# Performance work log

Measured on AMD Instinct MI355X. Metric: run time of the kernel, lower is better.

## Reference

```python
import jax, jax.numpy as jnp
import numpy as np

QMIN, QMAX = 0.0, 255.0  # uint8 activation quantization range


def _qlinear(x, w_q, b, s_in, zp_in, s_w):
    """zentorch_qlinear: quantize fp32 x to uint8, int8 weight, dequant output.

    x:   [M, K] fp32
    w_q: [N, K] int8 values (stored int32), symmetric (weight zp = 0)
    b:   [N] fp32
    s_in, zp_in: scalars (activation scale / zero point)
    s_w: [N] per-output-channel weight scales
    """
    zp = zp_in.astype(jnp.float32)
    q = jnp.clip(jnp.round(x / s_in) + zp, QMIN, QMAX)      # fake-quant uint8
    x_dq = (q - zp) * s_in                                   # dequantized activation
    w_dq = w_q.astype(jnp.float32) * s_w[:, None]            # [N, K] dequant weight
    return x_dq @ w_dq.T + b                                 # [M, N] fp32


def setup_inputs() -> dict:
    key = jax.random.key(0)
    k1, k2, k3, k4 = jax.random.split(key, 4)
    M, K, N = 8192, 4096, 4096
    inp = {
        "input": jax.random.normal(k1, (M, K), dtype=jnp.float32),
        "weights": jax.random.randint(k2, (N, K), -128, 128, dtype=jnp.int32),
        "biases": jax.random.normal(k3, (N,), dtype=jnp.float32) * 0.1,
        "input_scales": jnp.array([0.05], dtype=jnp.float32),
        "input_zero_points": jnp.array([128], dtype=jnp.int32),
        "weight_scales": jax.random.uniform(k4, (N,), dtype=jnp.float32, minval=0.001, maxval=0.01),
        "weight_zero_points": jnp.zeros((N,), dtype=jnp.int32),
        "output_dtype": 0,  # 0 -> float32
    }
    return inp


def reference(input, weights, biases, input_scales, input_zero_points,
              weight_scales, weight_zero_points, output_dtype):
    s_in = input_scales[0]
    zp_in = input_zero_points[0]
    x = _qlinear(input, weights, biases, s_in, zp_in, weight_scales)
    x = _qlinear(x, weights, biases, s_in, zp_in, weight_scales)
    x = _qlinear(x, weights, biases, s_in, zp_in, weight_scales)
    return x
```

## Files before the change

kernel.cpp:

```cpp
#include <hip/hip_runtime.h>
#include <stdint.h>

#define M_DIM 8192
#define K_DIM 4096
#define N_DIM 4096
#define KTILES (K_DIM / 64)

typedef __attribute__((ext_vector_type(4))) int i32x4;

__global__ void pack_w_kernel(const int* __restrict__ w, char* __restrict__ wp,
                              int* __restrict__ corr, const int* __restrict__ zpp) {
  __shared__ int red[256];
  const int n = blockIdx.x;
  const int t = threadIdx.x;
  const int4* row = (const int4*)(w + (size_t)n * K_DIM);
  int s = 0;
  int words[4];
#pragma unroll
  for (int u = 0; u < 4; ++u) {
    int4 v = row[t * 4 + u];
    s += v.x + v.y + v.z + v.w;
    words[u] = (v.x & 255) | ((v.y & 255) << 8) | ((v.z & 255) << 16) | (v.w << 24);
  }
  ((int4*)(wp + (size_t)n * K_DIM))[t] = make_int4(words[0], words[1], words[2], words[3]);
  red[t] = s;
  __syncthreads();
  for (int off = 128; off > 0; off >>= 1) {
    if (t < off) red[t] += red[t + off];
    __syncthreads();
  }
  if (t == 0) corr[n] = (128 - zpp[0]) * red[0];
}

__global__ void quant_in_kernel(const float* __restrict__ x, char* __restrict__ q,
                                const float* __restrict__ sp, const int* __restrict__ zpp) {
  const int i = blockIdx.x * blockDim.x + threadIdx.x;
  const float s = sp[0];
  const float zp = (float)zpp[0];
  float4 v = ((const float4*)x)[i];
  float t0 = fminf(fmaxf(rintf(v.x / s) + zp, 0.f), 255.f);
  float t1 = fminf(fmaxf(rintf(v.y / s) + zp, 0.f), 255.f);
  float t2 = fminf(fmaxf(rintf(v.z / s) + zp, 0.f), 255.f);
  float t3 = fminf(fmaxf(rintf(v.w / s) + zp, 0.f), 255.f);
  int b0 = (int)t0 - 128, b1 = (int)t1 - 128, b2 = (int)t2 - 128, b3 = (int)t3 - 128;
  ((int*)q)[i] = (b0 & 255) | ((b1 & 255) << 8) | ((b2 & 255) << 16) | (b3 << 24);
}

#define STAGE16(SRC, DST)                                                     \
  __builtin_amdgcn_global_load_lds(                                           \
      (const __attribute__((address_space(1))) void*)(SRC),                   \
      (__attribute__((address_space(3))) void*)(DST), 16, 0, 0)

#define RD(p) (*(const i32x4*)(p))

#define BAR __builtin_amdgcn_s_barrier()
#define LGKM0 asm volatile("s_waitcnt lgkmcnt(0)" ::: "memory")
#define SCHED0 __builtin_amdgcn_sched_barrier(0)

#define MF8(I0, AV, J0, BV)                                                   \
  _Pragma("unroll") for (int i_ = 0; i_ < 4; ++i_)                            \
      _Pragma("unroll") for (int j_ = 0; j_ < 2; ++j_)                        \
          acc[(I0) + i_][(J0) + j_] = __builtin_amdgcn_mfma_i32_16x16x64_i8(  \
              AV[i_], BV[j_], acc[(I0) + i_][(J0) + j_], 0, 0, 0);

#define TILE8(SLOT, KSTG)                                                     \
  {                                                                           \
    const char* sA_ = &lds[SLOT][0][0];                                       \
    const char* sB_ = &lds[SLOT][1][0];                                       \
    char* nA_ = &lds[((SLOT) + 3) & 3][0][0];                                 \
    char* nB_ = &lds[((SLOT) + 3) & 3][1][0];                                 \
    i32x4 aL[4], aH[4], bL[2], bH[2];                                         \
                                             \
    _Pragma("unroll") for (int i_ = 0; i_ < 4; ++i_)                          \
        aL[i_] = RD(sA_ + aoff[i_]);                                          \
    bL[0] = RD(sB_ + boff[0]);                                                \
    bL[1] = RD(sB_ + boff[1]);                                                \
    STAGE16(asrc0 + (size_t)(KSTG), nA_ + o0_);                               \
    BAR; LGKM0; SCHED0;                                                       \
    __builtin_amdgcn_s_setprio(1); MF8(0, aL, 0, bL)                          \
    __builtin_amdgcn_s_setprio(0);                                            \
    BAR;                                                                      \
                                             \
    bH[0] = RD(sB_ + boff[2]);                                                \
    bH[1] = RD(sB_ + boff[3]);                                                \
    STAGE16(asrc1 + (size_t)(KSTG), nA_ + o1_);                               \
    BAR; LGKM0; SCHED0;                                                       \
    __builtin_amdgcn_s_setprio(1); MF8(0, aL, 2, bH)                          \
    __builtin_amdgcn_s_setprio(0);                                            \
    BAR;                                                                      \
                                             \
    _Pragma("unroll") for (int i_ = 0; i_ < 4; ++i_)                          \
        aH[i_] = RD(sA_ + aoff[4 + i_]);                                      \
    STAGE16(bsrc0 + (size_t)(KSTG), nB_ + o0_);                               \
    BAR; LGKM0; SCHED0;                                                       \
    __builtin_amdgcn_s_setprio(1); MF8(4, aH, 2, bH)                          \
    __builtin_amdgcn_s_setprio(0);                                            \
    BAR;                                                                      \
                                  \
    STAGE16(bsrc1 + (size_t)(KSTG), nB_ + o1_);                               \
    BAR; SCHED0;                                                              \
    __builtin_amdgcn_s_setprio(1); MF8(4, aH, 0, bL)                          \
    __builtin_amdgcn_s_setprio(0);                                            \
    asm volatile("s_waitcnt vmcnt(8)" ::: "memory");                          \
    BAR;                                                                      \
  }

template <int WRITE_Q>
__global__ __launch_bounds__(512, 2) void gemm_kernel(
    const char* __restrict__ qa, const char* __restrict__ wb,
    const int* __restrict__ corr, const float* __restrict__ swp,
    const float* __restrict__ bias, const float* __restrict__ sp,
    const int* __restrict__ zpp, char* __restrict__ outq, float* __restrict__ outf) {
  __shared__ __align__(16) char lds[4][2][16384];
  const int tid = threadIdx.x;
  const int lane = tid & 63;
  const int w = tid >> 6;
  const int wr = w >> 2;
  const int wc = w & 3;
  const int bid = blockIdx.x;
  const int bm = bid & 31;
  const int bn = bid >> 5;
  const char* abase = qa + (size_t)bm * 256 * K_DIM;
  const char* bbase = wb + (size_t)bn * 256 * K_DIM;

  const int o0_ = tid * 16;
  const int o1_ = 8192 + tid * 16;
  const int r0_ = o0_ >> 6, r1_ = o1_ >> 6;
  const int g0_ = ((o0_ >> 4) & 3) ^ ((r0_ >> 1) & 3);
  const int g1_ = ((o1_ >> 4) & 3) ^ ((r1_ >> 1) & 3);
  const char* asrc0 = abase + (size_t)r0_ * K_DIM + g0_ * 16;
  const char* asrc1 = abase + (size_t)r1_ * K_DIM + g1_ * 16;
  const int p0_ = (r0_ & ~63) + 4 * (r0_ & 15) + ((r0_ >> 4) & 3);
  const int p1_ = (r1_ & ~63) + 4 * (r1_ & 15) + ((r1_ >> 4) & 3);
  const char* bsrc0 = bbase + (size_t)p0_ * K_DIM + g0_ * 16;
  const char* bsrc1 = bbase + (size_t)p1_ * K_DIM + g1_ * 16;

  const int rr = lane & 15;
  const int g = lane >> 4;
  int aoff[8], boff[4];
#pragma unroll
  for (int i = 0; i < 8; ++i) {
    const int row = wr * 128 + i * 16 + rr;
    aoff[i] = (row << 6) + ((g ^ ((row >> 1) & 3)) << 4);
  }
#pragma unroll
  for (int j = 0; j < 4; ++j) {
    const int row = wc * 64 + j * 16 + rr;
    boff[j] = (row << 6) + ((g ^ ((row >> 1) & 3)) << 4);
  }

  i32x4 acc[8][4] = {};

  STAGE16(asrc0, &lds[0][0][o0_]); STAGE16(asrc1, &lds[0][0][o1_]);
  STAGE16(bsrc0, &lds[0][1][o0_]); STAGE16(bsrc1, &lds[0][1][o1_]);
  STAGE16(asrc0 + 64, &lds[1][0][o0_]); STAGE16(asrc1 + 64, &lds[1][0][o1_]);
  STAGE16(bsrc0 + 64, &lds[1][1][o0_]); STAGE16(bsrc1 + 64, &lds[1][1][o1_]);
  STAGE16(asrc0 + 128, &lds[2][0][o0_]); STAGE16(asrc1 + 128, &lds[2][0][o1_]);
  STAGE16(bsrc0 + 128, &lds[2][1][o0_]); STAGE16(bsrc1 + 128, &lds[2][1][o1_]);
  asm volatile("s_waitcnt vmcnt(8)" ::: "memory");
  __builtin_amdgcn_s_barrier();

  for (int tb = 0; tb < KTILES / 4; ++tb) {
#pragma unroll
    for (int u = 0; u < 4; ++u) {
      const int t = tb * 4 + u;
      const int ks_ = (t + 3 < KTILES ? t + 3 : KTILES - 1) * 64;
      TILE8(u, ks_);
    }
  }
  asm volatile("s_waitcnt vmcnt(0)" ::: "memory");

  const float s = sp[0];
  const float zpf = (float)zpp[0];
  const int m0 = bm * 256 + wr * 128 + (lane >> 4) * 4;
  const int nb4 = bn * 256 + wc * 64 + ((lane & 15) << 2);
  const int4 cr4 = *(const int4*)(corr + nb4);
  const float4 sw4 = *(const float4*)(swp + nb4);
  const float4 bb4 = *(const float4*)(bias + nb4);
  const float fs0 = s * sw4.x, fs1 = s * sw4.y, fs2 = s * sw4.z, fs3 = s * sw4.w;
#pragma unroll
  for (int i = 0; i < 8; ++i) {
#pragma unroll
    for (int q = 0; q < 4; ++q) {
      const int m = m0 + i * 16 + q;
      const float v0 = fs0 * (float)(acc[i][0][q] + cr4.x) + bb4.x;
      const float v1 = fs1 * (float)(acc[i][1][q] + cr4.y) + bb4.y;
      const float v2 = fs2 * (float)(acc[i][2][q] + cr4.z) + bb4.z;
      const float v3 = fs3 * (float)(acc[i][3][q] + cr4.w) + bb4.w;
      if (WRITE_Q) {
        const int b0i = (int)fminf(fmaxf(rintf(v0 / s) + zpf, 0.f), 255.f) - 128;
        const int b1i = (int)fminf(fmaxf(rintf(v1 / s) + zpf, 0.f), 255.f) - 128;
        const int b2i = (int)fminf(fmaxf(rintf(v2 / s) + zpf, 0.f), 255.f) - 128;
        const int b3i = (int)fminf(fmaxf(rintf(v3 / s) + zpf, 0.f), 255.f) - 128;
        const uint32_t pk = (uint32_t)(b0i & 255) | ((uint32_t)(b1i & 255) << 8) |
                            ((uint32_t)(b2i & 255) << 16) | ((uint32_t)b3i << 24);
        *(uint32_t*)(outq + (size_t)m * N_DIM + nb4) = pk;
      } else {
        float4 o4;
        o4.x = v0; o4.y = v1; o4.z = v2; o4.w = v3;
        *(float4*)(outf + (size_t)m * N_DIM + nb4) = o4;
      }
    }
  }
}

extern "C" void kernel_launch(void* const* d_in, const int* in_sizes, int n_in,
                              void* d_out, int out_size, void* d_ws, size_t ws_size,
                              hipStream_t stream) {
  const float* x = (const float*)d_in[0];
  const int* wq = (const int*)d_in[1];
  const float* bias = (const float*)d_in[2];
  const float* s_in = (const float*)d_in[3];
  const int* zp_in = (const int*)d_in[4];
  const float* s_w = (const float*)d_in[5];
  float* out = (float*)d_out;

  const size_t WP_BYTES = (size_t)N_DIM * K_DIM;
  const size_t Q_BYTES = (size_t)M_DIM * K_DIM;
  char* ws = (char*)d_ws;
  char* wp = ws;
  char* q1 = ws + WP_BYTES;
  char* q2 = q1 + Q_BYTES;
  int* corr = (int*)(q2 + Q_BYTES);
  const size_t NEEDED = WP_BYTES + 2 * Q_BYTES + (size_t)N_DIM * sizeof(int);
  if (ws_size < NEEDED) return;

  pack_w_kernel<<<N_DIM, 256, 0, stream>>>(wq, wp, corr, zp_in);
  quant_in_kernel<<<(M_DIM * K_DIM / 4) / 256, 256, 0, stream>>>(x, q1, s_in, zp_in);

  dim3 grid((M_DIM / 256) * (N_DIM / 256));
  dim3 blk(512);
  gemm_kernel<1><<<grid, blk, 0, stream>>>(q1, wp, corr, s_w, bias, s_in, zp_in, q2, nullptr);
  gemm_kernel<1><<<grid, blk, 0, stream>>>(q2, wp, corr, s_w, bias, s_in, zp_in, q1, nullptr);
  gemm_kernel<0><<<grid, blk, 0, stream>>>(q1, wp, corr, s_w, bias, s_in, zp_in, nullptr, out);
}
```

Measured before the change: 442.0 us.

## Register ping-pong prefetch with one barrier per k-tile and swizzled block order

The four-phase k-tile body, with a barrier and an lgkmcnt wait around every MFMA group, is replaced by a two-half tile. The next tile's A/B fragments are prefetched from LDS into alternating register sets while the current tile's MFMAs run, so each k-tile now needs one vmcnt(4) wait and one barrier. The aim is to cut barrier stalls and expose more LDS-read latency overlap, at the cost of more live registers under launch_bounds(512,2). The block index is also remapped so that concurrently running blocks share A and B panels in L2.

```diff
diff --git a/kernel.cpp b/kernel.cpp
--- a/kernel.cpp
+++ b/kernel.cpp
@@ -53,56 +53,40 @@
 
 #define RD(p) (*(const i32x4*)(p))
 
-#define BAR __builtin_amdgcn_s_barrier()
-#define LGKM0 asm volatile("s_waitcnt lgkmcnt(0)" ::: "memory")
-#define SCHED0 __builtin_amdgcn_sched_barrier(0)
-
-#define MF8(I0, AV, J0, BV)                                                   \
-  _Pragma("unroll") for (int i_ = 0; i_ < 4; ++i_)                            \
-      _Pragma("unroll") for (int j_ = 0; j_ < 2; ++j_)                        \
-          acc[(I0) + i_][(J0) + j_] = __builtin_amdgcn_mfma_i32_16x16x64_i8(  \
-              AV[i_], BV[j_], acc[(I0) + i_][(J0) + j_], 0, 0, 0);
-
-#define TILE8(SLOT, KSTG)                                                     \
+#define TILE_PP(SLOT, KSTG, CA, CB, NA, NB, DO_NEXT)                          \
   {                                                                           \
-    const char* sA_ = &lds[SLOT][0][0];                                       \
-    const char* sB_ = &lds[SLOT][1][0];                                       \
+    const char* bufA_ = &lds[SLOT][0][0];                                     \
     char* nA_ = &lds[((SLOT) + 3) & 3][0][0];                                 \
     char* nB_ = &lds[((SLOT) + 3) & 3][1][0];                                 \
-    i32x4 aL[4], aH[4], bL[2], bH[2];                                         \
-                                             \
+    i32x4 a1_[4];                                                             \
     _Pragma("unroll") for (int i_ = 0; i_ < 4; ++i_)                          \
-        aL[i_] = RD(sA_ + aoff[i_]);                                          \
-    bL[0] = RD(sB_ + boff[0]);                                                \
-    bL[1] = RD(sB_ + boff[1]);                                                \
+        a1_[i_] = RD(bufA_ + aoff[4 + i_]);                                   \
     STAGE16(asrc0 + (size_t)(KSTG), nA_ + o0_);                               \
-    BAR; LGKM0; SCHED0;                                                       \
-    __builtin_amdgcn_s_setprio(1); MF8(0, aL, 0, bL)                          \
+    STAGE16(asrc1 + (size_t)(KSTG), nA_ + o1_);                               \
+    __builtin_amdgcn_s_setprio(1);                                            \
+    _Pragma("unroll") for (int i_ = 0; i_ < 4; ++i_)                          \
+        _Pragma("unroll") for (int j_ = 0; j_ < 4; ++j_)                      \
+            acc[i_][j_] = __builtin_amdgcn_mfma_i32_16x16x64_i8(              \
+                CA[i_], CB[j_], acc[i_][j_], 0, 0, 0);                        \
     __builtin_amdgcn_s_setprio(0);                                            \
-    BAR;                                                                      \
-                                             \
-    bH[0] = RD(sB_ + boff[2]);                                                \
-    bH[1] = RD(sB_ + boff[3]);                                                \
-    STAGE16(asrc1 + (size_t)(KSTG), nA_ + o1_);                               \
-    BAR; LGKM0; SCHED0;                                                       \
-    __builtin_amdgcn_s_setprio(1); MF8(0, aL, 2, bH)                          \
+    if (DO_NEXT) {                                                            \
+      const char* xA_ = &lds[((SLOT) + 1) & 3][0][0];                         \
+      const char* xB_ = &lds[((SLOT) + 1) & 3][1][0];                         \
+      _Pragma("unroll") for (int i_ = 0; i_ < 4; ++i_)                        \
+          NA[i_] = RD(xA_ + aoff[i_]);                                        \
+      _Pragma("unroll") for (int j_ = 0; j_ < 4; ++j_)                        \
+          NB[j_] = RD(xB_ + boff[j_]);                                        \
+    }                                                                         \
+    STAGE16(bsrc0 + (size_t)(KSTG), nB_ + o0_);                               \
+    STAGE16(bsrc1 + (size_t)(KSTG), nB_ + o1_);                               \
+    __builtin_amdgcn_s_setprio(1);                                            \
+    _Pragma("unroll") for (int i_ = 0; i_ < 4; ++i_)                          \
+        _Pragma("unroll") for (int j_ = 0; j_ < 4; ++j_)                      \
+            acc[4 + i_][j_] = __builtin_amdgcn_mfma_i32_16x16x64_i8(          \
+                a1_[i_], CB[j_], acc[4 + i_][j_], 0, 0, 0);                   \
     __builtin_amdgcn_s_setprio(0);                                            \
-    BAR;                                                                      \
-                                             \
-    _Pragma("unroll") for (int i_ = 0; i_ < 4; ++i_)                          \
-        aH[i_] = RD(sA_ + aoff[4 + i_]);                                      \
-    STAGE16(bsrc0 + (size_t)(KSTG), nB_ + o0_);                               \
-    BAR; LGKM0; SCHED0;                                                       \
-    __builtin_amdgcn_s_setprio(1); MF8(4, aH, 2, bH)                          \
-    __builtin_amdgcn_s_setprio(0);                                            \
-    BAR;                                                                      \
-                                  \
-    STAGE16(bsrc1 + (size_t)(KSTG), nB_ + o1_);                               \
-    BAR; SCHED0;                                                              \
-    __builtin_amdgcn_s_setprio(1); MF8(4, aH, 0, bL)                          \
-    __builtin_amdgcn_s_setprio(0);                                            \
-    asm volatile("s_waitcnt vmcnt(8)" ::: "memory");                          \
-    BAR;                                                                      \
+    asm volatile("s_waitcnt vmcnt(4)" ::: "memory");                          \
+    __builtin_amdgcn_s_barrier();                                             \
   }
 
 template <int WRITE_Q>
@@ -117,7 +101,8 @@
   const int w = tid >> 6;
   const int wr = w >> 2;
   const int wc = w & 3;
-  const int bid = blockIdx.x;
+  const int bid0 = blockIdx.x;
+  const int bid = (bid0 & 7) * 64 + (bid0 >> 3);
   const int bm = bid & 31;
   const int bn = bid >> 5;
   const char* abase = qa + (size_t)bm * 256 * K_DIM;
@@ -157,17 +142,26 @@
   STAGE16(bsrc0 + 64, &lds[1][1][o0_]); STAGE16(bsrc1 + 64, &lds[1][1][o1_]);
   STAGE16(asrc0 + 128, &lds[2][0][o0_]); STAGE16(asrc1 + 128, &lds[2][0][o1_]);
   STAGE16(bsrc0 + 128, &lds[2][1][o0_]); STAGE16(bsrc1 + 128, &lds[2][1][o1_]);
-  asm volatile("s_waitcnt vmcnt(8)" ::: "memory");
+  asm volatile("s_waitcnt vmcnt(4)" ::: "memory");
   __builtin_amdgcn_s_barrier();
 
-  for (int tb = 0; tb < KTILES / 4; ++tb) {
-#pragma unroll
-    for (int u = 0; u < 4; ++u) {
-      const int t = tb * 4 + u;
-      const int ks_ = (t + 3 < KTILES ? t + 3 : KTILES - 1) * 64;
-      TILE8(u, ks_);
-    }
-  }
+  i32x4 aA[4], bA[4], aB[4], bB[4];
+#pragma unroll
+  for (int i = 0; i < 4; ++i) aA[i] = RD(&lds[0][0][0] + aoff[i]);
+#pragma unroll
+  for (int j = 0; j < 4; ++j) bA[j] = RD(&lds[0][1][0] + boff[j]);
+
+  for (int tb = 0; tb < (KTILES - 4) / 4; ++tb) {
+    const int t0 = tb * 4;
+    TILE_PP(0, (size_t)(t0 + 3) * 64, aA, bA, aB, bB, 1)
+    TILE_PP(1, (size_t)(t0 + 4) * 64, aB, bB, aA, bA, 1)
+    TILE_PP(2, (size_t)(t0 + 5) * 64, aA, bA, aB, bB, 1)
+    TILE_PP(3, (size_t)(t0 + 6) * 64, aB, bB, aA, bA, 1)
+  }
+  TILE_PP(0, (size_t)(KTILES - 1) * 64, aA, bA, aB, bB, 1)
+  TILE_PP(1, (size_t)(KTILES - 1) * 64, aB, bB, aA, bA, 1)
+  TILE_PP(2, (size_t)(KTILES - 1) * 64, aA, bA, aB, bB, 1)
+  TILE_PP(3, (size_t)(KTILES - 1) * 64, aB, bB, aA, bA, 0)
   asm volatile("s_waitcnt vmcnt(0)" ::: "memory");
 
   const float s = sp[0];
```

Measured after the change: 461.5 us. +4.4%, slower.
